# Performance work log

Hardware: AMD Instinct MI355X
Metric: run time of the kernel (lower is better)

The kernel has to match this reference:

```python
import jax, jax.numpy as jnp
import numpy as np

B, L, D, DFF = 4, 4096, 1024, 4096
EPS = 1e-6

def _rmsnorm(x, w):
    return x * jax.lax.rsqrt(jnp.mean(x * x, axis=-1, keepdims=True) + EPS) * w

def setup_inputs() -> dict:
    key = jax.random.key(0)
    ks = jax.random.split(key, 16)
    s = 1.0 / np.sqrt(D)
    sf = 1.0 / np.sqrt(DFF)
    return {
        "x": jax.random.normal(ks[0], (B, L, D), jnp.float32),
        # QuasiLSTM gate linears, stored [in, out]; y = x @ W + b
        "w_forget": jax.random.normal(ks[1], (D, D), jnp.float32) * s,
        "b_forget": jnp.zeros((D,), jnp.float32),
        "w_input": jax.random.normal(ks[2], (D, D), jnp.float32) * s,
        "b_input": jnp.zeros((D,), jnp.float32),
        "w_igate": jax.random.normal(ks[3], (D, D), jnp.float32) * s,
        "b_igate": jnp.zeros((D,), jnp.float32),
        "w_ogate": jax.random.normal(ks[4], (D, D), jnp.float32) * s,
        "b_ogate": jnp.zeros((D,), jnp.float32),
        "h0": jax.random.normal(ks[5], (D,), jnp.float32),  # last_hidden_init
        "norm1_w": jnp.ones((D,), jnp.float32),
        "norm2_w": jnp.ones((D,), jnp.float32),
        # FFN SwiGLU
        "w_fc": jax.random.normal(ks[6], (D, DFF), jnp.float32) * s,
        "b_fc": jnp.zeros((DFF,), jnp.float32),
        "w_fc_act": jax.random.normal(ks[7], (D, DFF), jnp.float32) * s,
        "b_fc_act": jnp.zeros((DFF,), jnp.float32),
        "w_out": jax.random.normal(ks[8], (DFF, D), jnp.float32) * sf,
        "b_out": jnp.zeros((D,), jnp.float32),
    }

def reference(x, w_forget, b_forget, w_input, b_input, w_igate, b_igate,
              w_ogate, b_ogate, h0, norm1_w, norm2_w,
              w_fc, b_fc, w_fc_act, b_fc_act, w_out, b_out):
    # --- QuasiLSTM branch (pre-norm residual) ---
    x_res = x
    xn = _rmsnorm(x, norm1_w)                                   # [B,L,D]
    forget = jax.nn.sigmoid(xn @ w_forget + b_forget)           # a_t
    inp = jnp.tanh(xn @ w_input + b_input) * jax.nn.sigmoid(xn @ w_igate + b_igate)  # b_t
    # Linear recurrence h_t = a_t * h_{t-1} + b_t, h_0 = 0 (inner chunk),
    # computed as an associative scan over the length axis.
    def comb(left, right):
        a_l, b_l = left
        a_r, b_r = right
        return (a_l * a_r, b_l * a_r + b_r)
    _, h_inner = jax.lax.associative_scan(comb, (forget, inp), axis=1)
    # cross-chunk contribution from last_hidden_init
    h = h_inner + h0[None, None, :] * jnp.cumprod(forget, axis=1)
    y = jnp.tanh(h) * jax.nn.sigmoid(xn @ w_ogate + b_ogate)
    x1 = y + x_res  # dropout p=0 -> identity
    # --- FFN SwiGLU branch ---
    xn2 = _rmsnorm(x1, norm2_w)
    hff = (xn2 @ w_fc + b_fc) * jax.nn.silu(xn2 @ w_fc_act + b_fc_act)
    out = hff @ w_out + b_out
    return out + x1
```

## Files before the change

kernel.cpp:

```cpp
#include <hip/hip_runtime.h>
#include <math.h>
#include <stdint.h>

static constexpr int Bb  = 4;
static constexpr int Ll  = 4096;
static constexpr int Dd  = 1024;
static constexpr int DFF = 4096;
static constexpr int Mm  = Bb * Ll;
static constexpr int CH  = 64;
static constexpr int CS  = Ll / CH;
static constexpr float EPS = 1e-6f;

typedef __attribute__((ext_vector_type(8))) short short8;
typedef __attribute__((ext_vector_type(4))) float floatx4;
typedef __attribute__((ext_vector_type(4))) unsigned short us4;

__device__ __forceinline__ float sigmoidf_(float v) { return 1.0f / (1.0f + __expf(-v)); }
__device__ __forceinline__ float fast_tanh(float x) {
    return 2.0f / (1.0f + __expf(-2.0f * x)) - 1.0f;
}
__device__ __forceinline__ ushort f2bf(float f) {
    union { float f; uint32_t u; } v; v.f = f;
    return (ushort)((v.u + 0x7FFFu + ((v.u >> 16) & 1u)) >> 16);
}
__device__ __forceinline__ float bf2f(ushort h) {
    union { uint32_t u; float f; } v; v.u = (uint32_t)h << 16; return v.f;
}

__device__ __forceinline__ void gload16(const ushort* g, ushort* l) {
    __builtin_amdgcn_global_load_lds(
        (const __attribute__((address_space(1))) uint32_t*)g,
        (__attribute__((address_space(3))) uint32_t*)l, 16, 0, 0);
}

static constexpr int HT_US  = 256 * 32;
static constexpr int BUF_US = 4 * HT_US;

__device__ __forceinline__ void gemm_core_8ph(
    const ushort* __restrict__ A, const ushort* __restrict__ B1,
    const ushort* __restrict__ B2, int m0, int n0b1, int n0b2, int K,
    ushort* lds, floatx4 (&acc1)[8][2], floatx4 (&acc2)[8][2])
{
    const int tid = threadIdx.x;
    const int mm = tid >> 2, ss = tid & 3;
    const int kb = ss ^ ((mm >> 1) & 3);
    const ushort* pA0 = A  + (size_t)(m0 + mm) * K + kb * 8;
    const ushort* pA1 = pA0 + (size_t)128 * K;
    const ushort* pB0 = B1 + (size_t)(n0b1 + mm) * K + kb * 8;
    const ushort* pB1 = B2 + (size_t)(n0b2 + mm) * K + kb * 8;

    const int wave = tid >> 6, lane = tid & 63;
    const int wr = wave >> 2, wc = wave & 3;
    const int fr = lane & 15, q = lane >> 4;
    const int slot8 = (q ^ ((fr >> 1) & 3)) << 3;
    const int aoff  = (wr * 128 + fr) * 32 + slot8;
    const int boff  = 2 * HT_US + (wc * 32 + fr) * 32 + slot8;

    const int NT = K >> 6;

#define STG_A(bsel, kk, tt) do { \
        ushort* d_ = lds + (bsel) * BUF_US + (kk) * HT_US; \
        int o_ = (tt) * 64 + (kk) * 32; \
        gload16(pA0 + o_, d_ + tid * 8); \
        gload16(pA1 + o_, d_ + (tid + 512) * 8); } while (0)
#define STG_B(bsel, kk, tt) do { \
        ushort* d_ = lds + (bsel) * BUF_US + (2 + (kk)) * HT_US; \
        int o_ = (tt) * 64 + (kk) * 32; \
        gload16(pB0 + o_, d_ + tid * 8); \
        gload16(pB1 + o_, d_ + (tid + 512) * 8); } while (0)
#define MFMA_HALF(mh) do { \
        __builtin_amdgcn_s_setprio(1); \
        _Pragma("unroll") \
        for (int i_ = 0; i_ < 4; ++i_) { \
            acc1[(mh)*4+i_][0] = __builtin_amdgcn_mfma_f32_16x16x32_bf16(a[i_], b[0], acc1[(mh)*4+i_][0], 0, 0, 0); \
            acc2[(mh)*4+i_][0] = __builtin_amdgcn_mfma_f32_16x16x32_bf16(a[i_], c[0], acc2[(mh)*4+i_][0], 0, 0, 0); \
            acc1[(mh)*4+i_][1] = __builtin_amdgcn_mfma_f32_16x16x32_bf16(a[i_], b[1], acc1[(mh)*4+i_][1], 0, 0, 0); \
            acc2[(mh)*4+i_][1] = __builtin_amdgcn_mfma_f32_16x16x32_bf16(a[i_], c[1], acc2[(mh)*4+i_][1], 0, 0, 0); \
        } \
        __builtin_amdgcn_s_setprio(0); } while (0)
#define CLOSE_BAR() do { __builtin_amdgcn_sched_barrier(0); __builtin_amdgcn_s_barrier(); } while (0)

    STG_A(0, 0, 0); STG_B(0, 0, 0); STG_A(0, 1, 0); STG_B(0, 1, 0);
    asm volatile("s_waitcnt vmcnt(4)" ::: "memory");
    CLOSE_BAR();

    for (int t = 0; t < NT; ++t) {
        const int buf = t & 1, nbuf = buf ^ 1;
        const bool pf = (t + 1 < NT);
        const ushort* Ab = lds + buf * BUF_US;
        short8 a[4], b[2], c[2];

        #pragma unroll
        for (int i = 0; i < 4; ++i) a[i] = *(const short8*)&Ab[aoff + i * 512];
        #pragma unroll
        for (int n = 0; n < 2; ++n) {
            b[n] = *(const short8*)&Ab[boff + n * 512];
            c[n] = *(const short8*)&Ab[boff + 4096 + n * 512];
        }
        if (pf) STG_A(nbuf, 0, t + 1);
        __builtin_amdgcn_s_barrier();
        MFMA_HALF(0);
        CLOSE_BAR();

        #pragma unroll
        for (int i = 0; i < 4; ++i) a[i] = *(const short8*)&Ab[aoff + (i + 4) * 512];
        if (pf) STG_B(nbuf, 0, t + 1);
        __builtin_amdgcn_s_barrier();
        MFMA_HALF(1);
        if (pf) asm volatile("s_waitcnt vmcnt(4)" ::: "memory");
        else    asm volatile("s_waitcnt vmcnt(0)" ::: "memory");
        CLOSE_BAR();

        const ushort* Ab1 = Ab + HT_US;
        #pragma unroll
        for (int i = 0; i < 4; ++i) a[i] = *(const short8*)&Ab1[aoff + i * 512];
        #pragma unroll
        for (int n = 0; n < 2; ++n) {
            b[n] = *(const short8*)&Ab1[boff + n * 512];
            c[n] = *(const short8*)&Ab1[boff + 4096 + n * 512];
        }
        if (pf) STG_A(nbuf, 1, t + 1);
        __builtin_amdgcn_s_barrier();
        MFMA_HALF(0);
        CLOSE_BAR();

        #pragma unroll
        for (int i = 0; i < 4; ++i) a[i] = *(const short8*)&Ab1[aoff + (i + 4) * 512];
        if (pf) STG_B(nbuf, 1, t + 1);
        __builtin_amdgcn_s_barrier();
        MFMA_HALF(1);
        if (pf) asm volatile("s_waitcnt vmcnt(4)" ::: "memory");
        CLOSE_BAR();
    }
#undef STG_A
#undef STG_B
#undef MFMA_HALF
#undef CLOSE_BAR
}

__global__ __launch_bounds__(512) void mfma_gemm_gates(
    const ushort* __restrict__ A, const ushort* __restrict__ W1t,
    const ushort* __restrict__ W2t,
    const float* __restrict__ b_input, const float* __restrict__ b_forget,
    const float* __restrict__ b_igate, const float* __restrict__ b_ogate,
    ushort* __restrict__ Ga, ushort* __restrict__ Gb, ushort* __restrict__ Gog)
{
    __shared__ __align__(16) ushort lds[2 * BUF_US];
    int xcd = blockIdx.x & 7, i = blockIdx.x >> 3;
    int bx = xcd * 2 + (i & 1), by = i >> 1;
    int m0 = by * 256, n0 = bx * 128;

    floatx4 acc1[8][2] = {};
    floatx4 acc2[8][2] = {};
    gemm_core_8ph(A, W1t, W2t, m0, n0, n0, Dd, lds, acc1, acc2);

    int tid = threadIdx.x, wave = tid >> 6, lane = tid & 63;
    int wr = wave >> 2, wc = wave & 3, fr = lane & 15, q = lane >> 4;
    #pragma unroll
    for (int ni = 0; ni < 2; ++ni) {
        int col = n0 + wc * 32 + ni * 16 + fr;
        if (col < 1024) {
            float b1v = b_input[col], b2v = b_igate[col];
            #pragma unroll
            for (int mi = 0; mi < 8; ++mi)
                #pragma unroll
                for (int r = 0; r < 4; ++r) {
                    int row = m0 + wr * 128 + mi * 16 + q * 4 + r;
                    float z1 = acc1[mi][ni][r] + b1v;
                    float z2 = acc2[mi][ni][r] + b2v;
                    Gb[(size_t)row * Dd + col] = f2bf(fast_tanh(z1) * sigmoidf_(z2));
                }
        } else {
            int c2 = col - 1024;
            float b1v = b_forget[c2], b2v = b_ogate[c2];
            #pragma unroll
            for (int mi = 0; mi < 8; ++mi)
                #pragma unroll
                for (int r = 0; r < 4; ++r) {
                    int row = m0 + wr * 128 + mi * 16 + q * 4 + r;
                    float z1 = acc1[mi][ni][r] + b1v;
                    float z2 = acc2[mi][ni][r] + b2v;
                    Ga[(size_t)row * Dd + c2]  = f2bf(sigmoidf_(z1));
                    Gog[(size_t)row * Dd + c2] = f2bf(sigmoidf_(z2));
                }
        }
    }
}

__global__ __launch_bounds__(512) void mfma_gemm_swiglu(
    const ushort* __restrict__ A, const ushort* __restrict__ W1t,
    const float* __restrict__ b1, const ushort* __restrict__ W2t,
    const float* __restrict__ b2, ushort* __restrict__ C)
{
    __shared__ __align__(16) ushort lds[2 * BUF_US];
    int xcd = blockIdx.x & 7, i = blockIdx.x >> 3;
    int bx = xcd * 4 + (i & 3), by = i >> 2;
    int m0 = by * 256, n0 = bx * 128;

    floatx4 acc1[8][2] = {};
    floatx4 acc2[8][2] = {};
    gemm_core_8ph(A, W1t, W2t, m0, n0, n0, Dd, lds, acc1, acc2);

    int tid = threadIdx.x, wave = tid >> 6, lane = tid & 63;
    int wr = wave >> 2, wc = wave & 3, fr = lane & 15, q = lane >> 4;
    #pragma unroll
    for (int ni = 0; ni < 2; ++ni) {
        int col = n0 + wc * 32 + ni * 16 + fr;
        float b1v = b1[col], b2v = b2[col];
        #pragma unroll
        for (int mi = 0; mi < 8; ++mi)
            #pragma unroll
            for (int r = 0; r < 4; ++r) {
                int row = m0 + wr * 128 + mi * 16 + q * 4 + r;
                float z1 = acc1[mi][ni][r] + b1v;
                float z2 = acc2[mi][ni][r] + b2v;
                C[(size_t)row * DFF + col] = f2bf(z1 * z2 * sigmoidf_(z2));
            }
    }
}

__global__ __launch_bounds__(512) void mfma_gemm_residual(
    const ushort* __restrict__ A, const ushort* __restrict__ Wt,
    const float* __restrict__ bias, float* __restrict__ C)
{
    __shared__ __align__(16) ushort lds[2 * BUF_US];
    int xcd = blockIdx.x & 7, i = blockIdx.x >> 3;
    int s = xcd * 32 + i;
    int bx = s & 3, by = s >> 2;
    int m0 = by * 256, n0 = bx * 256;

    floatx4 acc1[8][2] = {};
    floatx4 acc2[8][2] = {};
    gemm_core_8ph(A, Wt, Wt, m0, n0, n0 + 128, DFF, lds, acc1, acc2);

    int tid = threadIdx.x, wave = tid >> 6, lane = tid & 63;
    int wr = wave >> 2, wc = wave & 3, fr = lane & 15, q = lane >> 4;
    #pragma unroll
    for (int ni = 0; ni < 2; ++ni) {
        int col1 = n0 + wc * 32 + ni * 16 + fr;
        int col2 = col1 + 128;
        float bs1 = bias[col1], bs2 = bias[col2];
        #pragma unroll
        for (int mi = 0; mi < 8; ++mi)
            #pragma unroll
            for (int r = 0; r < 4; ++r) {
                int row = m0 + wr * 128 + mi * 16 + q * 4 + r;
                size_t i1 = (size_t)row * Dd + col1;
                size_t i2 = (size_t)row * Dd + col2;
                C[i1] = acc1[mi][ni][r] + bs1 + C[i1];
                C[i2] = acc2[mi][ni][r] + bs2 + C[i2];
            }
    }
}

__global__ __launch_bounds__(256) void transpose_cast_kernel(
    const float* __restrict__ W, ushort* __restrict__ Wt, int K, int N)
{
    __shared__ float t[32][33];
    int lx = threadIdx.x & 31, ly = threadIdx.x >> 5;
    int n = blockIdx.x * 32 + lx;
    #pragma unroll
    for (int i = 0; i < 4; ++i) {
        int k = blockIdx.y * 32 + ly + i * 8;
        t[ly + i * 8][lx] = W[(size_t)k * N + n];
    }
    __syncthreads();
    int k2 = blockIdx.y * 32 + lx;
    #pragma unroll
    for (int i = 0; i < 4; ++i) {
        int n2 = blockIdx.x * 32 + ly + i * 8;
        Wt[(size_t)n2 * K + k2] = f2bf(t[lx][ly + i * 8]);
    }
}

__global__ __launch_bounds__(256) void transpose_cast_gates(
    const float* __restrict__ w_i, const float* __restrict__ w_f,
    const float* __restrict__ w_g, const float* __restrict__ w_o,
    ushort* __restrict__ W1t, ushort* __restrict__ W2t)
{
    int z = blockIdx.z;
    const float* W = (z == 0) ? w_i : (z == 1) ? w_f : (z == 2) ? w_g : w_o;
    ushort* Wt = (z == 0) ? W1t : (z == 1) ? W1t + (size_t)1024 * Dd
               : (z == 2) ? W2t : W2t + (size_t)1024 * Dd;
    __shared__ float t[32][33];
    int lx = threadIdx.x & 31, ly = threadIdx.x >> 5;
    int n = blockIdx.x * 32 + lx;
    #pragma unroll
    for (int i = 0; i < 4; ++i) {
        int k = blockIdx.y * 32 + ly + i * 8;
        t[ly + i * 8][lx] = W[(size_t)k * Dd + n];
    }
    __syncthreads();
    int k2 = blockIdx.y * 32 + lx;
    #pragma unroll
    for (int i = 0; i < 4; ++i) {
        int n2 = blockIdx.x * 32 + ly + i * 8;
        Wt[(size_t)n2 * Dd + k2] = f2bf(t[lx][ly + i * 8]);
    }
}

__global__ __launch_bounds__(256) void rmsnorm_bf16_kernel(
    const float* __restrict__ x, const float* __restrict__ w,
    ushort* __restrict__ o)
{
    int row = blockIdx.x;
    int tid = threadIdx.x;
    float4 v = ((const float4*)(x + (size_t)row * Dd))[tid];
    float ss = v.x*v.x + v.y*v.y + v.z*v.z + v.w*v.w;
    #pragma unroll
    for (int off = 32; off > 0; off >>= 1) ss += __shfl_down(ss, off, 64);
    __shared__ float red[4];
    if ((tid & 63) == 0) red[tid >> 6] = ss;
    __syncthreads();
    float scale = rsqrtf((red[0] + red[1] + red[2] + red[3]) * (1.0f / Dd) + EPS);
    float4 wv = ((const float4*)w)[tid];
    us4 ov;
    ov.x = f2bf(v.x * scale * wv.x);
    ov.y = f2bf(v.y * scale * wv.y);
    ov.z = f2bf(v.z * scale * wv.z);
    ov.w = f2bf(v.w * scale * wv.w);
    *(us4*)&o[(size_t)row * Dd + tid * 4] = ov;
}

__global__ __launch_bounds__(256) void scan_pass1(
    const ushort* __restrict__ Ga, const ushort* __restrict__ Gb,
    float* __restrict__ P, float* __restrict__ Hend)
{
    int tid = threadIdx.x;
    int c = blockIdx.x, b = blockIdx.y;
    size_t base = ((size_t)b * Ll + (size_t)c * CS) * Dd + tid * 4;
    float p[4] = {1.f, 1.f, 1.f, 1.f};
    float h[4] = {};
    #pragma unroll 4
    for (int t = 0; t < CS; ++t) {
        us4 av = *(const us4*)&Ga[base + (size_t)t * Dd];
        us4 bv = *(const us4*)&Gb[base + (size_t)t * Dd];
        #pragma unroll
        for (int j = 0; j < 4; ++j) {
            float aa = bf2f(av[j]);
            float bb = bf2f(bv[j]);
            p[j] *= aa;
            h[j] = aa * h[j] + bb;
        }
    }
    size_t o = ((size_t)b * CH + c) * Dd + tid * 4;
    *(float4*)&P[o]    = make_float4(p[0], p[1], p[2], p[3]);
    *(float4*)&Hend[o] = make_float4(h[0], h[1], h[2], h[3]);
}

__global__ __launch_bounds__(256) void scan_pass2(
    const float* __restrict__ P, const float* __restrict__ Hend,
    const float* __restrict__ h0, float* __restrict__ Carry)
{
    int idx = blockIdx.x * 256 + threadIdx.x;
    int b = idx / Dd, d = idx % Dd;
    float carry = h0[d];
    for (int c = 0; c < CH; ++c) {
        size_t o = ((size_t)b * CH + c) * Dd + d;
        Carry[o] = carry;
        carry = P[o] * carry + Hend[o];
    }
}

__global__ __launch_bounds__(256) void scan_pass3_norm(
    const ushort* __restrict__ Ga, const ushort* __restrict__ Gb,
    const ushort* __restrict__ Gog, const float* __restrict__ Carry,
    const float* __restrict__ x, const float* __restrict__ norm2w,
    float* __restrict__ x1, ushort* __restrict__ xnb)
{
    int tid = threadIdx.x;
    int c = blockIdx.x, b = blockIdx.y;
    size_t base = ((size_t)b * Ll + (size_t)c * CS) * Dd + tid * 4;
    float4 h4 = *(const float4*)&Carry[((size_t)b * CH + c) * Dd + tid * 4];
    float h[4] = {h4.x, h4.y, h4.z, h4.w};
    float4 w4 = ((const float4*)norm2w)[tid];
    float wv[4] = {w4.x, w4.y, w4.z, w4.w};
    __shared__ float red[4];

    for (int t = 0; t < CS; ++t) {
        size_t i = base + (size_t)t * Dd;
        us4 av = *(const us4*)&Ga[i];
        us4 bv = *(const us4*)&Gb[i];
        us4 gv = *(const us4*)&Gog[i];
        float4 xv = *(const float4*)&x[i];
        float xs[4] = {xv.x, xv.y, xv.z, xv.w};
        float v[4];
        #pragma unroll
        for (int j = 0; j < 4; ++j) {
            float aa = bf2f(av[j]);
            float bb = bf2f(bv[j]);
            h[j] = aa * h[j] + bb;
            v[j] = fast_tanh(h[j]) * bf2f(gv[j]) + xs[j];
        }
        *(float4*)&x1[i] = make_float4(v[0], v[1], v[2], v[3]);
        float ss = v[0]*v[0] + v[1]*v[1] + v[2]*v[2] + v[3]*v[3];
        #pragma unroll
        for (int off = 32; off > 0; off >>= 1) ss += __shfl_down(ss, off, 64);
        if ((tid & 63) == 0) red[tid >> 6] = ss;
        __syncthreads();
        float scale = rsqrtf((red[0] + red[1] + red[2] + red[3]) * (1.0f / Dd) + EPS);
        us4 ov;
        #pragma unroll
        for (int j = 0; j < 4; ++j) ov[j] = f2bf(v[j] * scale * wv[j]);
        *(us4*)&xnb[i] = ov;
        __syncthreads();
    }
}

extern "C" void kernel_launch(void* const* d_in, const int* in_sizes, int n_in,
                              void* d_out, int out_size, void* d_ws, size_t ws_size,
                              hipStream_t stream)
{
    const float* x        = (const float*)d_in[0];
    const float* w_forget = (const float*)d_in[1];
    const float* b_forget = (const float*)d_in[2];
    const float* w_input  = (const float*)d_in[3];
    const float* b_input  = (const float*)d_in[4];
    const float* w_igate  = (const float*)d_in[5];
    const float* b_igate  = (const float*)d_in[6];
    const float* w_ogate  = (const float*)d_in[7];
    const float* b_ogate  = (const float*)d_in[8];
    const float* h0       = (const float*)d_in[9];
    const float* norm1_w  = (const float*)d_in[10];
    const float* norm2_w  = (const float*)d_in[11];
    const float* w_fc     = (const float*)d_in[12];
    const float* b_fc     = (const float*)d_in[13];
    const float* w_fc_act = (const float*)d_in[14];
    const float* b_fc_act = (const float*)d_in[15];
    const float* w_out    = (const float*)d_in[16];
    const float* b_out    = (const float*)d_in[17];
    float* out = (float*)d_out;

    char* ws = (char*)d_ws;
    const size_t MB = 1ull << 20;
    ushort* wtG1  = (ushort*)(ws + 0 * MB);
    ushort* wtG2  = (ushort*)(ws + 4 * MB);
    ushort* wtFC  = (ushort*)(ws + 8 * MB);
    ushort* wtFCA = (ushort*)(ws + 16 * MB);
    ushort* wtOUT = (ushort*)(ws + 24 * MB);
    ushort* xnb   = (ushort*)(ws + 32 * MB);
    ushort* Ga    = (ushort*)(ws + 64 * MB);
    ushort* Gb    = (ushort*)(ws + 96 * MB);
    ushort* Gog   = (ushort*)(ws + 128 * MB);
    ushort* hff   = (ushort*)(ws + 64 * MB);
    float*  P     = (float*)(ws + 192 * MB);
    float*  Hend  = (float*)(ws + 193 * MB);
    float*  Carry = (float*)(ws + 194 * MB);

    transpose_cast_gates<<<dim3(32, 32, 4), 256, 0, stream>>>(
        w_input, w_forget, w_igate, w_ogate, wtG1, wtG2);
    transpose_cast_kernel<<<dim3(DFF/32, Dd/32), 256, 0, stream>>>(w_fc,     wtFC,  Dd, DFF);
    transpose_cast_kernel<<<dim3(DFF/32, Dd/32), 256, 0, stream>>>(w_fc_act, wtFCA, Dd, DFF);
    transpose_cast_kernel<<<dim3(Dd/32, DFF/32), 256, 0, stream>>>(w_out,    wtOUT, DFF, Dd);

    rmsnorm_bf16_kernel<<<Mm, 256, 0, stream>>>(x, norm1_w, xnb);

    mfma_gemm_gates<<<(2048/128) * (Mm/256), 512, 0, stream>>>(
        xnb, wtG1, wtG2, b_input, b_forget, b_igate, b_ogate, Ga, Gb, Gog);

    dim3 sg(CH, Bb);
    scan_pass1<<<sg, 256, 0, stream>>>(Ga, Gb, P, Hend);
    scan_pass2<<<(Bb * Dd) / 256, 256, 0, stream>>>(P, Hend, h0, Carry);
    scan_pass3_norm<<<sg, 256, 0, stream>>>(Ga, Gb, Gog, Carry, x, norm2_w,
                                            out, xnb);

    mfma_gemm_swiglu<<<(DFF/128) * (Mm/256), 512, 0, stream>>>(
        xnb, wtFC, b_fc, wtFCA, b_fc_act, hff);

    mfma_gemm_residual<<<(Dd/256) * (Mm/256), 512, 0, stream>>>(
        hff, wtOUT, b_out, out);
}
```

Baseline: 853.8 us.

## Software-pipeline scan_pass3 norm, use wave-per-row rmsnorm, merge FFN weight transposes

scan_pass3_norm now packs two chunks per 512-thread block and double-buffers the row-sum reduction slots. The next timestep's loads and recurrence are computed before the barrier, so each step needs one __syncthreads instead of two. rmsnorm_bf16_kernel now handles one row per wavefront using xor shuffles and no shared-memory barrier, scan_pass2 launches 64-thread blocks to spread its 4096 threads over more CUs, and the two FFN weight transposes are merged into one launch. Together these cut barrier stalls and launch overhead in the small elementwise kernels. The trade-off is more register pressure in the pass-3 kernel, and the 2x64 grid is still small.

After: 859.8 us. About the same (+0.7%).

```diff
diff --git a/kernel.cpp b/kernel.cpp
--- a/kernel.cpp
+++ b/kernel.cpp
@@ -273,6 +273,29 @@
     }
 }
 
+__global__ __launch_bounds__(256) void transpose_cast_ffn(
+    const float* __restrict__ w_fc, const float* __restrict__ w_fc_act,
+    ushort* __restrict__ wtFC, ushort* __restrict__ wtFCA)
+{
+    const float* W = blockIdx.z ? w_fc_act : w_fc;
+    ushort* Wt = blockIdx.z ? wtFCA : wtFC;
+    __shared__ float t[32][33];
+    int lx = threadIdx.x & 31, ly = threadIdx.x >> 5;
+    int n = blockIdx.x * 32 + lx;
+    #pragma unroll
+    for (int i = 0; i < 4; ++i) {
+        int k = blockIdx.y * 32 + ly + i * 8;
+        t[ly + i * 8][lx] = W[(size_t)k * DFF + n];
+    }
+    __syncthreads();
+    int k2 = blockIdx.y * 32 + lx;
+    #pragma unroll
+    for (int i = 0; i < 4; ++i) {
+        int n2 = blockIdx.x * 32 + ly + i * 8;
+        Wt[(size_t)n2 * Dd + k2] = f2bf(t[lx][ly + i * 8]);
+    }
+}
+
 __global__ __launch_bounds__(256) void transpose_cast_gates(
     const float* __restrict__ w_i, const float* __restrict__ w_f,
     const float* __restrict__ w_g, const float* __restrict__ w_o,
@@ -303,23 +326,29 @@
     const float* __restrict__ x, const float* __restrict__ w,
     ushort* __restrict__ o)
 {
-    int row = blockIdx.x;
-    int tid = threadIdx.x;
-    float4 v = ((const float4*)(x + (size_t)row * Dd))[tid];
-    float ss = v.x*v.x + v.y*v.y + v.z*v.z + v.w*v.w;
-    #pragma unroll
-    for (int off = 32; off > 0; off >>= 1) ss += __shfl_down(ss, off, 64);
-    __shared__ float red[4];
-    if ((tid & 63) == 0) red[tid >> 6] = ss;
-    __syncthreads();
-    float scale = rsqrtf((red[0] + red[1] + red[2] + red[3]) * (1.0f / Dd) + EPS);
-    float4 wv = ((const float4*)w)[tid];
-    us4 ov;
-    ov.x = f2bf(v.x * scale * wv.x);
-    ov.y = f2bf(v.y * scale * wv.y);
-    ov.z = f2bf(v.z * scale * wv.z);
-    ov.w = f2bf(v.w * scale * wv.w);
-    *(us4*)&o[(size_t)row * Dd + tid * 4] = ov;
+    int wave = threadIdx.x >> 6, lane = threadIdx.x & 63;
+    int row = blockIdx.x * 4 + wave;
+    const float4* xr = (const float4*)(x + (size_t)row * Dd);
+    float4 v[4];
+    float ss = 0.f;
+    #pragma unroll
+    for (int j = 0; j < 4; ++j) {
+        v[j] = xr[lane + j * 64];
+        ss += v[j].x * v[j].x + v[j].y * v[j].y + v[j].z * v[j].z + v[j].w * v[j].w;
+    }
+    #pragma unroll
+    for (int off = 1; off < 64; off <<= 1) ss += __shfl_xor(ss, off, 64);
+    float scale = rsqrtf(ss * (1.0f / Dd) + EPS);
+    #pragma unroll
+    for (int j = 0; j < 4; ++j) {
+        float4 wv = ((const float4*)w)[lane + j * 64];
+        us4 ov;
+        ov.x = f2bf(v[j].x * scale * wv.x);
+        ov.y = f2bf(v[j].y * scale * wv.y);
+        ov.z = f2bf(v[j].z * scale * wv.z);
+        ov.w = f2bf(v[j].w * scale * wv.w);
+        *(us4*)&o[(size_t)row * Dd + (lane + j * 64) * 4] = ov;
+    }
 }
 
 __global__ __launch_bounds__(256) void scan_pass1(
@@ -348,11 +377,11 @@
     *(float4*)&Hend[o] = make_float4(h[0], h[1], h[2], h[3]);
 }
 
-__global__ __launch_bounds__(256) void scan_pass2(
+__global__ __launch_bounds__(64) void scan_pass2(
     const float* __restrict__ P, const float* __restrict__ Hend,
     const float* __restrict__ h0, float* __restrict__ Carry)
 {
-    int idx = blockIdx.x * 256 + threadIdx.x;
+    int idx = blockIdx.x * 64 + threadIdx.x;
     int b = idx / Dd, d = idx % Dd;
     float carry = h0[d];
     for (int c = 0; c < CH; ++c) {
@@ -362,29 +391,29 @@
     }
 }
 
-__global__ __launch_bounds__(256) void scan_pass3_norm(
+__global__ __launch_bounds__(512) void scan_pass3_norm(
     const ushort* __restrict__ Ga, const ushort* __restrict__ Gb,
     const ushort* __restrict__ Gog, const float* __restrict__ Carry,
     const float* __restrict__ x, const float* __restrict__ norm2w,
     float* __restrict__ x1, ushort* __restrict__ xnb)
 {
     int tid = threadIdx.x;
-    int c = blockIdx.x, b = blockIdx.y;
-    size_t base = ((size_t)b * Ll + (size_t)c * CS) * Dd + tid * 4;
-    float4 h4 = *(const float4*)&Carry[((size_t)b * CH + c) * Dd + tid * 4];
+    int half = tid >> 8, ltid = tid & 255;
+    int c = blockIdx.x * 2 + half, b = blockIdx.y;
+    size_t base = ((size_t)b * Ll + (size_t)c * CS) * Dd + ltid * 4;
+    float4 h4 = *(const float4*)&Carry[((size_t)b * CH + c) * Dd + ltid * 4];
     float h[4] = {h4.x, h4.y, h4.z, h4.w};
-    float4 w4 = ((const float4*)norm2w)[tid];
+    float4 w4 = ((const float4*)norm2w)[ltid];
     float wv[4] = {w4.x, w4.y, w4.z, w4.w};
-    __shared__ float red[4];
-
-    for (int t = 0; t < CS; ++t) {
-        size_t i = base + (size_t)t * Dd;
-        us4 av = *(const us4*)&Ga[i];
-        us4 bv = *(const us4*)&Gb[i];
-        us4 gv = *(const us4*)&Gog[i];
-        float4 xv = *(const float4*)&x[i];
+    __shared__ float red[2][2][4];
+
+    float v[4];
+    {
+        us4 av = *(const us4*)&Ga[base];
+        us4 bv = *(const us4*)&Gb[base];
+        us4 gv = *(const us4*)&Gog[base];
+        float4 xv = *(const float4*)&x[base];
         float xs[4] = {xv.x, xv.y, xv.z, xv.w};
-        float v[4];
         #pragma unroll
         for (int j = 0; j < 4; ++j) {
             float aa = bf2f(av[j]);
@@ -392,17 +421,43 @@
             h[j] = aa * h[j] + bb;
             v[j] = fast_tanh(h[j]) * bf2f(gv[j]) + xs[j];
         }
-        *(float4*)&x1[i] = make_float4(v[0], v[1], v[2], v[3]);
+        *(float4*)&x1[base] = make_float4(v[0], v[1], v[2], v[3]);
         float ss = v[0]*v[0] + v[1]*v[1] + v[2]*v[2] + v[3]*v[3];
         #pragma unroll
         for (int off = 32; off > 0; off >>= 1) ss += __shfl_down(ss, off, 64);
-        if ((tid & 63) == 0) red[tid >> 6] = ss;
-        __syncthreads();
-        float scale = rsqrtf((red[0] + red[1] + red[2] + red[3]) * (1.0f / Dd) + EPS);
+        if ((ltid & 63) == 0) red[0][half][ltid >> 6] = ss;
+    }
+    __syncthreads();
+
+    for (int t = 0; t < CS; ++t) {
+        int p = t & 1;
+        float scale = rsqrtf((red[p][half][0] + red[p][half][1] +
+                              red[p][half][2] + red[p][half][3]) * (1.0f / Dd) + EPS);
         us4 ov;
         #pragma unroll
         for (int j = 0; j < 4; ++j) ov[j] = f2bf(v[j] * scale * wv[j]);
-        *(us4*)&xnb[i] = ov;
+        *(us4*)&xnb[base + (size_t)t * Dd] = ov;
+
+        if (t + 1 < CS) {
+            size_t i = base + (size_t)(t + 1) * Dd;
+            us4 av = *(const us4*)&Ga[i];
+            us4 bv = *(const us4*)&Gb[i];
+            us4 gv = *(const us4*)&Gog[i];
+            float4 xv = *(const float4*)&x[i];
+            float xs[4] = {xv.x, xv.y, xv.z, xv.w};
+            #pragma unroll
+            for (int j = 0; j < 4; ++j) {
+                float aa = bf2f(av[j]);
+                float bb = bf2f(bv[j]);
+                h[j] = aa * h[j] + bb;
+                v[j] = fast_tanh(h[j]) * bf2f(gv[j]) + xs[j];
+            }
+            *(float4*)&x1[i] = make_float4(v[0], v[1], v[2], v[3]);
+            float ss = v[0]*v[0] + v[1]*v[1] + v[2]*v[2] + v[3]*v[3];
+            #pragma unroll
+            for (int off = 32; off > 0; off >>= 1) ss += __shfl_down(ss, off, 64);
+            if ((ltid & 63) == 0) red[(t + 1) & 1][half][ltid >> 6] = ss;
+        }
         __syncthreads();
     }
 }
@@ -449,20 +504,20 @@
 
     transpose_cast_gates<<<dim3(32, 32, 4), 256, 0, stream>>>(
         w_input, w_forget, w_igate, w_ogate, wtG1, wtG2);
-    transpose_cast_kernel<<<dim3(DFF/32, Dd/32), 256, 0, stream>>>(w_fc,     wtFC,  Dd, DFF);
-    transpose_cast_kernel<<<dim3(DFF/32, Dd/32), 256, 0, stream>>>(w_fc_act, wtFCA, Dd, DFF);
-    transpose_cast_kernel<<<dim3(Dd/32, DFF/32), 256, 0, stream>>>(w_out,    wtOUT, DFF, Dd);
-
-    rmsnorm_bf16_kernel<<<Mm, 256, 0, stream>>>(x, norm1_w, xnb);
+    transpose_cast_ffn<<<dim3(DFF/32, Dd/32, 2), 256, 0, stream>>>(
+        w_fc, w_fc_act, wtFC, wtFCA);
+    transpose_cast_kernel<<<dim3(Dd/32, DFF/32), 256, 0, stream>>>(w_out, wtOUT, DFF, Dd);
+
+    rmsnorm_bf16_kernel<<<Mm / 4, 256, 0, stream>>>(x, norm1_w, xnb);
 
     mfma_gemm_gates<<<(2048/128) * (Mm/256), 512, 0, stream>>>(
         xnb, wtG1, wtG2, b_input, b_forget, b_igate, b_ogate, Ga, Gb, Gog);
 
     dim3 sg(CH, Bb);
     scan_pass1<<<sg, 256, 0, stream>>>(Ga, Gb, P, Hend);
-    scan_pass2<<<(Bb * Dd) / 256, 256, 0, stream>>>(P, Hend, h0, Carry);
-    scan_pass3_norm<<<sg, 256, 0, stream>>>(Ga, Gb, Gog, Carry, x, norm2_w,
-                                            out, xnb);
+    scan_pass2<<<(Bb * Dd) / 64, 64, 0, stream>>>(P, Hend, h0, Carry);
+    scan_pass3_norm<<<dim3(CH / 2, Bb), 512, 0, stream>>>(
+        Ga, Gb, Gog, Carry, x, norm2_w, out, xnb);
 
     mfma_gemm_swiglu<<<(DFF/128) * (Mm/256), 512, 0, stream>>>(
         xnb, wtFC, b_fc, wtFCA, b_fc_act, hff);
```
